# Optimization experiments

Hardware: AMD Instinct MI355X
Metric: run time of the kernel (lower is better)

The kernel has to match this reference:

```python
import jax, jax.numpy as jnp
import numpy as np

NUM_FIELDS = 26

def setup_inputs() -> dict:
    key = jax.random.key(0)
    ks = jax.random.split(key, 8)
    B, F, D, V, d, af = 4096, NUM_FIELDS, 13, 100000, 64, 64
    return {
        "sparse_feat": jax.random.randint(ks[0], (B, F), 0, V, dtype=jnp.int32),
        "dense_feat": jax.random.uniform(ks[1], (B, D), dtype=jnp.float32),
        "embed_table": jax.random.normal(ks[2], (V, d), dtype=jnp.float32) * 0.05,
        "lin_table": jax.random.normal(ks[3], (V,), dtype=jnp.float32) * 0.05,
        "w_dense": jax.random.normal(ks[4], (D,), dtype=jnp.float32) * 0.1,
        "bias": jnp.zeros((1,), dtype=jnp.float32),
        "W1": jax.random.normal(ks[5], (d, af), dtype=jnp.float32) * (1.0 / np.sqrt(d)),
        "b1": jnp.zeros((af,), dtype=jnp.float32),
        "w2": jax.random.normal(ks[6], (af,), dtype=jnp.float32) * (1.0 / np.sqrt(af)),
        "p": jax.random.normal(ks[7], (d,), dtype=jnp.float32) * (1.0 / np.sqrt(d)),
    }

def reference(sparse_feat, dense_feat, embed_table, lin_table, w_dense, bias, W1, b1, w2, p):
    # Embedding lookup: [B, F, d]
    emb = embed_table[sparse_feat]
    # Linear part: per-field scalar weights + dense linear + bias -> [B]
    linear_out = lin_table[sparse_feat].sum(axis=1) + dense_feat @ w_dense + bias[0]
    # Pairwise interactions i<j (static indices): [B, P, d]
    i_idx, j_idx = np.triu_indices(NUM_FIELDS, k=1)
    att_x = emb[:, i_idx, :] * emb[:, j_idx, :]
    # Attention MLP: Linear(d, af) + ReLU + Linear(af, 1, no bias) -> [B, P]
    h = jax.nn.relu(jnp.einsum('bpd,da->bpa', att_x, W1) + b1)
    att_w = jnp.einsum('bpa,a->bp', h, w2)
    att_score = jax.nn.softmax(att_w, axis=1)
    # Softmax-weighted sum over pairs -> [B, d], then final projection p -> [B]
    att_out = jnp.einsum('bpd,bp->bd', att_x, att_score)
    fm_att_out = att_out @ p
    return linear_out + fm_att_out
```

## Files before the change

kernel.cpp:

```cpp
#include <hip/hip_runtime.h>
#include <math.h>


#define NF 26
#define NP 325
#define NPP 336
#define NMT 21
#define ED 64
#define AF 64
#define NDENSE 13
#define WPB 4
#define BLOCK (WPB * 64)
#define ESTRIDE 72

typedef __attribute__((ext_vector_type(8))) _Float16 half8;
typedef __attribute__((ext_vector_type(4))) _Float16 half4;
typedef __attribute__((ext_vector_type(4))) float f32x4;

__device__ __forceinline__ void wsync() {
    __builtin_amdgcn_fence(__ATOMIC_ACQ_REL, "workgroup");
    __builtin_amdgcn_wave_barrier();
}

__global__ void prep_kernel(const float* __restrict__ W1,
                            _Float16* __restrict__ w1t,
                            unsigned short* __restrict__ tab)
{
    int t = threadIdx.x;
    for (int idx = t; idx < ED * AF; idx += 256) {
        int d = idx >> 6, a = idx & 63;
        w1t[a * ED + d] = (_Float16)W1[idx];
    }
    if (t < NPP) {
        unsigned short v = 0;
        if (t < NP) {
            int rem = t, i = 0;
            while (rem >= NF - 1 - i) { rem -= NF - 1 - i; ++i; }
            v = (unsigned short)(i | ((i + 1 + rem) << 8));
        }
        tab[t] = v;
    }
}

__global__ __launch_bounds__(BLOCK, 4)
void afm_kernel(const int*   __restrict__ sparse,
                const float* __restrict__ dense,
                const float* __restrict__ etab,
                const float* __restrict__ ltab,
                const float* __restrict__ wdense,
                const float* __restrict__ bias,
                const float* __restrict__ b1,
                const float* __restrict__ w2,
                const float* __restrict__ proj,
                const _Float16* __restrict__ w1t,
                const unsigned short* __restrict__ tab,
                float*       __restrict__ out,
                int B)
{
    const int t    = threadIdx.x;
    const int wave = t >> 6;
    const int lane = t & 63;
    const int qd   = lane >> 4;
    const int ln   = lane & 15;

    const int r = blockIdx.x * WPB + wave;
    if (r >= B) return;

    __shared__ alignas(16) _Float16 emb_all[WPB][NF][ESTRIDE];
    __shared__ alignas(16) float    sc_all[WPB][NPP];

    _Float16 (* __restrict__ emb)[ESTRIDE] = emb_all[wave];
    float* __restrict__ scores = sc_all[wave];

    half8 bfr[4][2];
    #pragma unroll
    for (int nt = 0; nt < 4; ++nt)
        #pragma unroll
        for (int kh = 0; kh < 2; ++kh)
            bfr[nt][kh] = *(const half8*)(w1t + (nt * 16 + ln) * ED + kh * 32 + qd * 8);

    float b1v[4], w2v[4];
    #pragma unroll
    for (int nt = 0; nt < 4; ++nt) {
        b1v[nt] = b1[nt * 16 + ln];
        w2v[nt] = w2[nt * 16 + ln];
    }

    const int* __restrict__ srow = sparse + r * NF;
    for (int task = lane; task < NF * 16; task += 64) {
        int f = task >> 4, q = task & 15;
        float4 v = *(const float4*)(etab + (size_t)srow[f] * ED + q * 4);
        half4 h = { (_Float16)v.x, (_Float16)v.y, (_Float16)v.z, (_Float16)v.w };
        *(half4*)(&emb[f][q * 4]) = h;
    }

    float lin = 0.f;
    if (lane < NF) {
        lin = ltab[srow[lane]];
    } else if (lane >= 32 && lane < 32 + NDENSE) {
        int k = lane - 32;
        lin = dense[r * NDENSE + k] * wdense[k];
    }
    #pragma unroll
    for (int off = 32; off >= 1; off >>= 1) lin += __shfl_xor(lin, off, 64);
    lin += bias[0];

    wsync();

    for (int mt = 0; mt < NMT; ++mt) {
        const int p0 = mt * 16 + ln;
        const unsigned pp = tab[p0];
        const int fi = pp & 0xff, fj = pp >> 8;

        half8 a0 = *(const half8*)(&emb[fi][qd * 8])      * *(const half8*)(&emb[fj][qd * 8]);
        half8 a1 = *(const half8*)(&emb[fi][32 + qd * 8]) * *(const half8*)(&emb[fj][32 + qd * 8]);

        float lg[4] = {0.f, 0.f, 0.f, 0.f};
        #pragma unroll
        for (int nt = 0; nt < 4; ++nt) {
            f32x4 acc = {0.f, 0.f, 0.f, 0.f};
            acc = __builtin_amdgcn_mfma_f32_16x16x32_f16(a0, bfr[nt][0], acc, 0, 0, 0);
            acc = __builtin_amdgcn_mfma_f32_16x16x32_f16(a1, bfr[nt][1], acc, 0, 0, 0);
            #pragma unroll
            for (int rr = 0; rr < 4; ++rr)
                lg[rr] = fmaf(fmaxf(acc[rr] + b1v[nt], 0.f), w2v[nt], lg[rr]);
        }
        #pragma unroll
        for (int off = 1; off <= 8; off <<= 1) {
            #pragma unroll
            for (int rr = 0; rr < 4; ++rr) lg[rr] += __shfl_xor(lg[rr], off, 64);
        }
        if (ln == 0) {
            const int pr = mt * 16 + qd * 4;
            float4 st;
            st.x = (pr + 0 < NP) ? lg[0] : -INFINITY;
            st.y = (pr + 1 < NP) ? lg[1] : -INFINITY;
            st.z = (pr + 2 < NP) ? lg[2] : -INFINITY;
            st.w = (pr + 3 < NP) ? lg[3] : -INFINITY;
            *(float4*)(&scores[pr]) = st;
        }
    }

    wsync();

    float v[6];
    #pragma unroll
    for (int k = 0; k < 6; ++k) {
        int p = lane + (k << 6);
        v[k] = (p < NPP) ? scores[p] : -INFINITY;
    }
    float m = v[0];
    #pragma unroll
    for (int k = 1; k < 6; ++k) m = fmaxf(m, v[k]);
    #pragma unroll
    for (int off = 32; off >= 1; off >>= 1) m = fmaxf(m, __shfl_xor(m, off, 64));
    float e[6], esum = 0.f;
    #pragma unroll
    for (int k = 0; k < 6; ++k) { e[k] = __expf(v[k] - m); esum += e[k]; }
    #pragma unroll
    for (int off = 32; off >= 1; off >>= 1) esum += __shfl_xor(esum, off, 64);
    const float rinv = 1.0f / esum;
    #pragma unroll
    for (int k = 0; k < 6; ++k) {
        int p = lane + (k << 6);
        if (p < NPP) scores[p] = e[k] * rinv;
    }

    wsync();

    const int dg  = lane & 7;
    const int sub = lane >> 3;
    half8 acc8 = { (_Float16)0.f, (_Float16)0.f, (_Float16)0.f, (_Float16)0.f,
                   (_Float16)0.f, (_Float16)0.f, (_Float16)0.f, (_Float16)0.f };
    for (int it = 0; it < NPP / 8; ++it) {
        const int p = it * 8 + sub;
        const float s = scores[p];
        const unsigned pp = tab[p];
        const int fi = pp & 0xff, fj = pp >> 8;
        const _Float16 sh = (_Float16)s;
        half8 sv = { sh, sh, sh, sh, sh, sh, sh, sh };
        half8 x = *(const half8*)(&emb[fi][dg * 8]) * *(const half8*)(&emb[fj][dg * 8]);
        acc8 += sv * x;
    }
    float av[8];
    #pragma unroll
    for (int i = 0; i < 8; ++i) av[i] = (float)acc8[i];
    #pragma unroll
    for (int off = 8; off <= 32; off <<= 1) {
        #pragma unroll
        for (int i = 0; i < 8; ++i) av[i] += __shfl_xor(av[i], off, 64);
    }
    float4 pa = *(const float4*)(proj + dg * 8);
    float4 pb = *(const float4*)(proj + dg * 8 + 4);
    float part = av[0] * pa.x + av[1] * pa.y + av[2] * pa.z + av[3] * pa.w
               + av[4] * pb.x + av[5] * pb.y + av[6] * pb.z + av[7] * pb.w;
    #pragma unroll
    for (int off = 1; off <= 4; off <<= 1) part += __shfl_xor(part, off, 64);

    if (lane == 0) out[r] = lin + part;
}

extern "C" void kernel_launch(void* const* d_in, const int* in_sizes, int n_in,
                              void* d_out, int out_size, void* d_ws, size_t ws_size,
                              hipStream_t stream) {
    const int*   sparse = (const int*)  d_in[0];
    const float* dense  = (const float*)d_in[1];
    const float* etab   = (const float*)d_in[2];
    const float* ltab   = (const float*)d_in[3];
    const float* wdense = (const float*)d_in[4];
    const float* bias   = (const float*)d_in[5];
    const float* W1     = (const float*)d_in[6];
    const float* b1     = (const float*)d_in[7];
    const float* w2     = (const float*)d_in[8];
    const float* proj   = (const float*)d_in[9];
    float* outp = (float*)d_out;

    _Float16*       w1t = (_Float16*)d_ws;
    unsigned short* tab = (unsigned short*)((char*)d_ws + 8192);

    const int B = in_sizes[0] / NF;

    prep_kernel<<<dim3(1), dim3(256), 0, stream>>>(W1, w1t, tab);
    afm_kernel<<<dim3((B + WPB - 1) / WPB), dim3(BLOCK), 0, stream>>>(
        sparse, dense, etab, ltab, wdense, bias, b1, w2, proj, w1t, tab, outp, B);
    (void)n_in; (void)out_size; (void)ws_size;
}
```

Baseline: 129.5 us.

## Split each batch row across two waves instead of one wave per row

Reorganizes the kernel so each 128-thread block processes a single batch row, with two waves sharing the embedding gather, the MFMA attention tiles and the weighted pair sum. A final cross-wave reduction goes through shared memory. The aim is to halve the per-row serial latency and raise the number of blocks in flight. In exchange it adds block-wide barriers, duplicates the softmax reduction in both waves, and loads the W1 fragments twice per row.

Result: slower. 168.4 us (+30.1%).

```diff
diff --git a/kernel.cpp b/kernel.cpp
--- a/kernel.cpp
+++ b/kernel.cpp
@@ -9,18 +9,12 @@
 #define ED 64
 #define AF 64
 #define NDENSE 13
-#define WPB 4
-#define BLOCK (WPB * 64)
+#define BLOCK 128
 #define ESTRIDE 72
 
 typedef __attribute__((ext_vector_type(8))) _Float16 half8;
 typedef __attribute__((ext_vector_type(4))) _Float16 half4;
 typedef __attribute__((ext_vector_type(4))) float f32x4;
-
-__device__ __forceinline__ void wsync() {
-    __builtin_amdgcn_fence(__ATOMIC_ACQ_REL, "workgroup");
-    __builtin_amdgcn_wave_barrier();
-}
 
 __global__ void prep_kernel(const float* __restrict__ W1,
                             _Float16* __restrict__ w1t,
@@ -42,7 +36,7 @@
     }
 }
 
-__global__ __launch_bounds__(BLOCK, 4)
+__global__ __launch_bounds__(BLOCK, 8)
 void afm_kernel(const int*   __restrict__ sparse,
                 const float* __restrict__ dense,
                 const float* __restrict__ etab,
@@ -54,23 +48,18 @@
                 const float* __restrict__ proj,
                 const _Float16* __restrict__ w1t,
                 const unsigned short* __restrict__ tab,
-                float*       __restrict__ out,
-                int B)
+                float*       __restrict__ out)
 {
     const int t    = threadIdx.x;
     const int wave = t >> 6;
     const int lane = t & 63;
     const int qd   = lane >> 4;
     const int ln   = lane & 15;
-
-    const int r = blockIdx.x * WPB + wave;
-    if (r >= B) return;
-
-    __shared__ alignas(16) _Float16 emb_all[WPB][NF][ESTRIDE];
-    __shared__ alignas(16) float    sc_all[WPB][NPP];
-
-    _Float16 (* __restrict__ emb)[ESTRIDE] = emb_all[wave];
-    float* __restrict__ scores = sc_all[wave];
+    const int r    = blockIdx.x;
+
+    __shared__ alignas(16) _Float16 emb[NF][ESTRIDE];
+    __shared__ alignas(16) float    scores[NPP];
+    __shared__ alignas(16) float    partial[2][ED];
 
     half8 bfr[4][2];
     #pragma unroll
@@ -87,7 +76,7 @@
     }
 
     const int* __restrict__ srow = sparse + r * NF;
-    for (int task = lane; task < NF * 16; task += 64) {
+    for (int task = t; task < NF * 16; task += BLOCK) {
         int f = task >> 4, q = task & 15;
         float4 v = *(const float4*)(etab + (size_t)srow[f] * ED + q * 4);
         half4 h = { (_Float16)v.x, (_Float16)v.y, (_Float16)v.z, (_Float16)v.w };
@@ -95,19 +84,21 @@
     }
 
     float lin = 0.f;
-    if (lane < NF) {
-        lin = ltab[srow[lane]];
-    } else if (lane >= 32 && lane < 32 + NDENSE) {
-        int k = lane - 32;
-        lin = dense[r * NDENSE + k] * wdense[k];
-    }
-    #pragma unroll
-    for (int off = 32; off >= 1; off >>= 1) lin += __shfl_xor(lin, off, 64);
-    lin += bias[0];
-
-    wsync();
-
-    for (int mt = 0; mt < NMT; ++mt) {
+    if (wave == 0) {
+        if (lane < NF) {
+            lin = ltab[srow[lane]];
+        } else if (lane >= 32 && lane < 32 + NDENSE) {
+            int k = lane - 32;
+            lin = dense[r * NDENSE + k] * wdense[k];
+        }
+        #pragma unroll
+        for (int off = 32; off >= 1; off >>= 1) lin += __shfl_xor(lin, off, 64);
+        lin += bias[0];
+    }
+
+    __syncthreads();
+
+    for (int mt = wave; mt < NMT; mt += 2) {
         const int p0 = mt * 16 + ln;
         const unsigned pp = tab[p0];
         const int fi = pp & 0xff, fj = pp >> 8;
@@ -141,7 +132,7 @@
         }
     }
 
-    wsync();
+    __syncthreads();
 
     float v[6];
     #pragma unroll
@@ -160,20 +151,23 @@
     #pragma unroll
     for (int off = 32; off >= 1; off >>= 1) esum += __shfl_xor(esum, off, 64);
     const float rinv = 1.0f / esum;
+    __syncthreads();
     #pragma unroll
     for (int k = 0; k < 6; ++k) {
-        int p = lane + (k << 6);
-        if (p < NPP) scores[p] = e[k] * rinv;
-    }
-
-    wsync();
+        if ((k >= wave * 3) && (k < wave * 3 + 3)) {
+            int p = lane + (k << 6);
+            if (p < NPP) scores[p] = e[k] * rinv;
+        }
+    }
+
+    __syncthreads();
 
     const int dg  = lane & 7;
-    const int sub = lane >> 3;
+    const int sub = (wave << 3) + (lane >> 3);
     half8 acc8 = { (_Float16)0.f, (_Float16)0.f, (_Float16)0.f, (_Float16)0.f,
                    (_Float16)0.f, (_Float16)0.f, (_Float16)0.f, (_Float16)0.f };
-    for (int it = 0; it < NPP / 8; ++it) {
-        const int p = it * 8 + sub;
+    for (int it = 0; it < NPP / 16; ++it) {
+        const int p = it * 16 + sub;
         const float s = scores[p];
         const unsigned pp = tab[p];
         const int fi = pp & 0xff, fj = pp >> 8;
@@ -190,14 +184,27 @@
         #pragma unroll
         for (int i = 0; i < 8; ++i) av[i] += __shfl_xor(av[i], off, 64);
     }
-    float4 pa = *(const float4*)(proj + dg * 8);
-    float4 pb = *(const float4*)(proj + dg * 8 + 4);
-    float part = av[0] * pa.x + av[1] * pa.y + av[2] * pa.z + av[3] * pa.w
-               + av[4] * pb.x + av[5] * pb.y + av[6] * pb.z + av[7] * pb.w;
-    #pragma unroll
-    for (int off = 1; off <= 4; off <<= 1) part += __shfl_xor(part, off, 64);
-
-    if (lane == 0) out[r] = lin + part;
+    if (lane < 8) {
+        *(float4*)(&partial[wave][lane * 8])     = make_float4(av[0], av[1], av[2], av[3]);
+        *(float4*)(&partial[wave][lane * 8 + 4]) = make_float4(av[4], av[5], av[6], av[7]);
+    }
+    __syncthreads();
+
+    if (wave == 0 && lane < 8) {
+        float4 s0 = *(const float4*)(&partial[0][lane * 8]);
+        float4 s1 = *(const float4*)(&partial[0][lane * 8 + 4]);
+        float4 t0 = *(const float4*)(&partial[1][lane * 8]);
+        float4 t1 = *(const float4*)(&partial[1][lane * 8 + 4]);
+        float4 pa = *(const float4*)(proj + lane * 8);
+        float4 pb = *(const float4*)(proj + lane * 8 + 4);
+        float part = (s0.x + t0.x) * pa.x + (s0.y + t0.y) * pa.y
+                   + (s0.z + t0.z) * pa.z + (s0.w + t0.w) * pa.w
+                   + (s1.x + t1.x) * pb.x + (s1.y + t1.y) * pb.y
+                   + (s1.z + t1.z) * pb.z + (s1.w + t1.w) * pb.w;
+        #pragma unroll
+        for (int off = 1; off <= 4; off <<= 1) part += __shfl_xor(part, off, 64);
+        if (lane == 0) out[r] = lin + part;
+    }
 }
 
 extern "C" void kernel_launch(void* const* d_in, const int* in_sizes, int n_in,
@@ -221,7 +228,7 @@
     const int B = in_sizes[0] / NF;
 
     prep_kernel<<<dim3(1), dim3(256), 0, stream>>>(W1, w1t, tab);
-    afm_kernel<<<dim3((B + WPB - 1) / WPB), dim3(BLOCK), 0, stream>>>(
-        sparse, dense, etab, ltab, wdense, bias, b1, w2, proj, w1t, tab, outp, B);
+    afm_kernel<<<dim3(B), dim3(BLOCK), 0, stream>>>(
+        sparse, dense, etab, ltab, wdense, bias, b1, w2, proj, w1t, tab, outp);
     (void)n_in; (void)out_size; (void)ws_size;
 }
```
